# Optimization experiments

Measured on AMD Instinct MI355X. Metric: run time of the kernel, lower is better.

## Reference

```python
import jax, jax.numpy as jnp
import numpy as np

ALPHA, BETA, LAMB, GAMMA = 1.0, 1.0, 1e-4, 1.0
K_NN, TAU = 50, 0.1
EPS = 1e-8


def _sqdist(A, B):
    # ||a - b||^2, clamped at 0 like the torch code
    d2 = (A * A).sum(1)[:, None] + (B * B).sum(1)[None, :] - 2.0 * (A @ B.T)
    return jnp.maximum(d2, 0.0)


def _mmd(s, t):
    comb = jnp.concatenate([s, t], axis=0)
    sigma_sq = jax.lax.stop_gradient(jnp.median(_sqdist(comb, comb))) / 2.0
    sigma_sq = jnp.where(sigma_sq < 1e-6, jnp.float32(1.0), sigma_sq)
    g = 1.0 / (sigma_sq + EPS)
    kxx = jnp.exp(-g * _sqdist(s, s)).mean()
    kyy = jnp.exp(-g * _sqdist(t, t)).mean()
    kxy = jnp.exp(-g * _sqdist(s, t)).mean()
    return jnp.maximum(kxx + kyy - 2.0 * kxy, 0.0)


def setup_inputs() -> dict:
    key = jax.random.key(0)
    ks = jax.random.split(key, 8)
    B, d, N, Nq, K = 256, 128, 200000, 10000, K_NN
    q_batch = jax.random.normal(ks[0], (B, d), jnp.float32)
    X = jax.random.normal(ks[1], (N, d), jnp.float32)
    W = jax.random.normal(ks[2], (d, d), jnp.float32) * (1.0 / np.sqrt(d))
    b = jnp.zeros((d,), jnp.float32)
    pre_weights = jax.random.uniform(ks[3], (Nq, K), jnp.float32)
    pre_weights = pre_weights / pre_weights.sum(1, keepdims=True)
    pre_indices = jax.random.randint(ks[4], (Nq, K), 0, N)
    q_indices = jax.random.randint(ks[5], (B,), 0, Nq)
    idx = jax.random.randint(ks[6], (B,), 0, N)
    return {"q_batch": q_batch, "X": X, "W": W, "b": b,
            "pre_weights": pre_weights, "pre_indices": pre_indices,
            "q_indices": q_indices, "idx": idx}


def reference(q_batch, X, W, b, pre_weights, pre_indices, q_indices, idx):
    Tq = q_batch @ W.T + b                                   # model(q_batch), Linear(d, d)
    # ---- MMD between mapped queries and a random database batch ----
    loss_dist = _mmd(Tq, X[idx])
    # ---- exact KNN (faiss IndexFlatL2 equivalent) on detached embeddings ----
    d2_all = _sqdist(jax.lax.stop_gradient(Tq), X)           # [B, N]
    _, post_idx = jax.lax.top_k(-d2_all, K_NN)               # [B, K] nearest neighbors
    Xn = X[post_idx]                                         # [B, K, d]
    l2 = ((Tq[:, None, :] - Xn) ** 2).sum(-1)                # [B, K] (grad flows here)
    post_w = jax.nn.softmax(-l2 / TAU, axis=1)
    # ---- union-KL, vectorized over batch (exact torch.unique semantics) ----
    pre_i = pre_indices[q_indices]                           # [B, K]
    pre_w = pre_weights[q_indices]                           # [B, K]
    cat = jnp.concatenate([pre_i, post_idx], axis=1)         # [B, 2K]
    # multiplicity of each id within the concatenated list -> collapse duplicates
    mult = (cat[:, :, None] == cat[:, None, :]).sum(-1).astype(jnp.float32)  # [B, 2K]
    p_raw = jnp.einsum('bmk,bk->bm',
                       (cat[:, :, None] == pre_i[:, None, :]).astype(jnp.float32), pre_w)
    q_raw = jnp.einsum('bmk,bk->bm',
                       (cat[:, :, None] == post_idx[:, None, :]).astype(jnp.float32), post_w)
    p_c = jnp.maximum(p_raw, EPS)
    q_c = jnp.maximum(q_raw, EPS)
    p = p_c / (p_c / mult).sum(1, keepdims=True)             # normalize over union
    q = q_c / (q_c / mult).sum(1, keepdims=True)
    kl = ((p * (jnp.log(p) - jnp.log(q))) / mult).sum(1)     # KL(p || q) per sample
    loss_knn = kl.mean()
    # ---- L2 regularization of model params & anchor loss ----
    loss_reg = 0.5 * ((W ** 2).sum() + (b ** 2).sum())
    loss_anchor = ((Tq - q_batch) ** 2).sum(1).mean()
    total = ALPHA * loss_dist + BETA * loss_knn + LAMB * loss_reg + GAMMA * loss_anchor
    return jnp.stack([total, loss_dist, loss_knn, loss_anchor])
```

## Files before the change

kernel.cpp:

```cpp
#include <hip/hip_runtime.h>
#include <cstdint>

#define D 128
#define NPTS 200000
#define KNN 50
#define CAP 8192
#define NS 8192
#define SLACK 2.0f
#define BAND 4.0f
#define EB 2048

#define OFF_ACC    0
#define OFF_SEL    256
#define OFF_CNT    1024
#define OFF_HIST0  17408
#define OFF_HIST12 148480
#define ZERO_BYTES 214016
#define OFF_COMB   214016
#define OFF_D2     476160
#define OFF_XN     1524736
#define OFF_SAMP   2324736
#define OFF_EBUF   2324736
#define OFF_THR    10713344
#define OFF_CANDI  10714368
#define OFF_SCO    19102976
#define OFF_TQSW   27491584
#define OFF_XBF    27557120
#define OFF_ANCP   78757120
#define OFF_WREGP  78758144
#define OFF_BCNT   78758400
#define OFF_KSA    78774272

typedef __attribute__((ext_vector_type(8))) short bf16x8;
typedef __attribute__((ext_vector_type(4))) float f32x4;
typedef const __attribute__((address_space(1))) void* gas_p;
typedef __attribute__((address_space(3))) void* las_p;

__device__ __forceinline__ unsigned fkey(float f) {
    unsigned u = __float_as_uint(f);
    return u ^ ((unsigned)((int)u >> 31) | 0x80000000u);
}

__device__ __forceinline__ void stage8k(const unsigned short* __restrict__ g,
                                        unsigned short* l, int w, int lane)
{
    #pragma unroll
    for (int j = 0; j < 2; j++) {
        const unsigned short* gp = g + j * 2048 + w * 512 + lane * 8;
        unsigned short* lp = l + j * 2048 + w * 512;
        __builtin_amdgcn_global_load_lds((gas_p)gp, (las_p)lp, 16, 0, 0);
    }
}

__global__ void k_phase1(const float* __restrict__ q, const float* __restrict__ X,
                         const float* __restrict__ W, const float* __restrict__ bb,
                         const int* __restrict__ idx, float* __restrict__ comb,
                         unsigned short* __restrict__ tqsw, unsigned short* __restrict__ xbf,
                         float* __restrict__ xn, float* __restrict__ ancp,
                         float* __restrict__ wregp, float* __restrict__ wszero)
{
    const int blk = blockIdx.x, t = threadIdx.x;
    if (blk < 12500) {
        __shared__ float xr4[4][16];
        const int lr = t & 15;
// ... 110 lines not shown
            const int r = (ck * 2 + tt) * 16 + lr;
            float xnv = xn[r];
            bf16x8 bfr[4];
            #pragma unroll
            for (int ks = 0; ks < 4; ks++)
                bfr[ks] = *(const bf16x8*)(sb + tt * 2048 + ks * 512 + lane * 8);
            f32x4 acc4[4];
            #pragma unroll
            for (int i = 0; i < 4; i++) acc4[i] = (f32x4){0.f, 0.f, 0.f, 0.f};
            #pragma unroll
            for (int ks = 0; ks < 4; ks++)
                #pragma unroll
                for (int i = 0; i < 4; i++)
                    acc4[i] = __builtin_amdgcn_mfma_f32_16x16x32_bf16(a[i][ks], bfr[ks], acc4[i], 0, 0, 0);
            #pragma unroll
            for (int i = 0; i < 4; i++)
                #pragma unroll
                for (int reg = 0; reg < 4; reg++) {
                    int qq = w * 64 + i * 16 + quad * 4 + reg;
                    samp[qq * NS + r] = xnv - 2.f * acc4[i][reg];
                }
        }
    }
}

__global__ void k_h1thr(const float* __restrict__ D2w, unsigned* __restrict__ hist12,
                        const unsigned* __restrict__ hist0, unsigned* __restrict__ sel,
                        const float* __restrict__ samp, float* __restrict__ thr)
{
    __shared__ unsigned buf[8192];
    __shared__ unsigned bins[4096];
    __shared__ unsigned part[256];
    __shared__ unsigned selll[4];
    __shared__ unsigned wred[4];
    const int t = threadIdx.x;
    if (blockIdx.x < 256) {
        unsigned s = 0;
        #pragma unroll
        for (int m = 0; m < 16; m++) {
            int bin = t * 16 + m;
            unsigned bs = 0;
            #pragma unroll
            for (int sh = 0; sh < 8; sh++) bs += hist0[bin * 8 + sh];
            bins[bin] = bs;
            s += bs;
        }
        part[t] = s;
        for (int m = t; m < 8192; m += 256) buf[m] = 0;
        __syncthreads();
        if (t == 0) {
            for (int tg = 0; tg < 2; tg++) {
                unsigned r = tg ? 131072u : 131071u;
                int c = 0;
                while (part[c] <= r) { r -= part[c]; c++; }
                int b = c * 16;
                while (bins[b] <= r) { r -= bins[b]; b++; }
                selll[2 * tg] = (unsigned)b; selll[2 * tg + 1] = r;
            }
            if (blockIdx.x == 0) {
                sel[0] = selll[0]; sel[1] = selll[1]; sel[2] = selll[2]; sel[3] = selll[3];
            }
        }
        __syncthreads();
        unsigned p0 = selll[0], p1 = selll[2];
        const int e0 = blockIdx.x * 1024;
        for (int m = 0; m < 4; m++) {
            unsigned key = __float_as_uint(D2w[e0 + m * 256 + t]);
            if ((key >> 20) == p0) atomicAdd(&buf[(key >> 8) & 0xFFFu], 1u);
            if ((key >> 20) == p1) atomicAdd(&buf[4096 + ((key >> 8) & 0xFFFu)], 1u);
        }
        __syncthreads();
        for (int m = t; m < 8192; m += 256) { unsigned v = buf[m]; if (v) atomicAdd(&hist12[m], v); }
    } else {
        const int q = blockIdx.x - 256;
        unsigned kreg[32];
        #pragma unroll
        for (int i = 0; i < 32; i++) kreg[i] = fkey(samp[q * NS + i * 256 + t]);
        unsigned v = 0;
        for (int bit = 31; bit >= 0; bit--) {
            unsigned trial = v | (1u << bit);
            unsigned c = 0;
            #pragma unroll
            for (int i = 0; i < 32; i++) c += (kreg[i] < trial) ? 1u : 0u;
            #pragma unroll
            for (int off = 32; off > 0; off >>= 1) c += __shfl_down(c, off);
            if ((t & 63) == 0) wred[t >> 6] = c;
            __syncthreads();
            unsigned total = wred[0] + wred[1] + wred[2] + wred[3];
            __syncthreads();
            if (total <= (unsigned)(KNN - 1)) v = trial;
        }
        if (t == 0) {
            unsigned orig = (v & 0x80000000u) ? (v ^ 0x80000000u) : ~v;
            thr[q] = __uint_as_float(orig) + SLACK;
        }
    }
}

#define FILT_BODY(SBUF)                                                              \
    do {                                                                             \
        _Pragma("unroll")                                                            \
        for (int tt = 0; tt < 2; tt++) {                                             \
            const int r = (ck * 2 + tt) * 16 + lr;                                   \
            float xnv = xn[r];                                                       \
            bf16x8 bv[4];                                                            \
            _Pragma("unroll")                                                        \
            for (int ks2 = 0; ks2 < 4; ks2++)                                        \
                bv[ks2] = *(const bf16x8*)(SBUF + tt * 2048 + ks2 * 512 + lane * 8); \
            f32x4 acc4[4];                                                           \
            _Pragma("unroll")                                                        \
            for (int i = 0; i < 4; i++) acc4[i] = (f32x4){0.f, 0.f, 0.f, 0.f};       \
            _Pragma("unroll")                                                        \
            for (int ks2 = 0; ks2 < 4; ks2++)                                        \
                _Pragma("unroll")                                                    \
                for (int i = 0; i < 4; i++)                                          \
                    acc4[i] = __builtin_amdgcn_mfma_f32_16x16x32_bf16(a[i][ks2], bv[ks2], acc4[i], 0, 0, 0); \
            _Pragma("unroll")                                                        \
            for (int i = 0; i < 4; i++)                                              \
                _Pragma("unroll")                                                    \
                for (int reg = 0; reg < 4; reg++) {                                  \
                    float s = xnv - 2.f * acc4[i][reg];                              \
                    if (s <= th_r[i][reg]) {                                         \
                        unsigned qq = (unsigned)(w * 64 + i * 16 + quad * 4 + reg);  \
                        unsigned p = atomicAdd(&lcnt, 1u);                           \
                        if (p < 1024u) { lbuf[p] = (qq << 18) | (unsigned)r; lsco[p] = fkey(s); } \
                        else {                                                       \
                            unsigned dd2 = gbase + p;                                \
                            if (dd2 < EB) { eb[dd2] = (qq << 18) | (unsigned)r; ebs[dd2] = fkey(s); } \
                        }                                                            \
                    }                                                                \
                }                                                                    \
        }                                                                            \
    } while (0)

__global__ __launch_bounds__(256) void k_filt2(const unsigned short* __restrict__ tqsw,
    const unsigned short* __restrict__ xbf, const float* __restrict__ xn,
    const float* __restrict__ thr, unsigned* __restrict__ ebuf, unsigned* __restrict__ esco,
    unsigned* __restrict__ bcnt, const float* __restrict__ D2w,
    unsigned* __restrict__ hist12, unsigned* __restrict__ sel)
{
    if (blockIdx.x >= 1024) {
        __shared__ unsigned h2c[512];
        __shared__ unsigned part2[256];
        __shared__ unsigned pfx[2];
        __shared__ unsigned rr[2];
        const int t = threadIdx.x;
        for (int tg = 0; tg < 2; tg++) {
            const unsigned* hh = hist12 + tg * 4096;
            unsigned s = 0;
            for (int m = 0; m < 16; m++) s += hh[t * 16 + m];
            part2[t] = s;
            __syncthreads();
            if (t == 0) {
                unsigned r = sel[1 + 2 * tg];
                int c = 0;
                while (part2[c] <= r) { r -= part2[c]; c++; }
                int b = c * 16;
                while (hh[b] <= r) { r -= hh[b]; b++; }
                pfx[tg] = (sel[2 * tg] << 12) | (unsigned)b;
                rr[tg] = r;
            }
            __syncthreads();
        }
        if (blockIdx.x == 1024 && t == 0) {
            sel[4] = pfx[0]; sel[5] = rr[0]; sel[6] = pfx[1]; sel[7] = rr[1];
        }
        h2c[t] = 0; h2c[256 + t] = 0;
        __syncthreads();
        unsigned p0 = pfx[0], p1 = pfx[1];
        const int e0 = (blockIdx.x - 1024) * 1024;
        for (int m = 0; m < 4; m++) {
            unsigned key = __float_as_uint(D2w[e0 + m * 256 + t]);
            if ((key >> 8) == p0) atomicAdd(&h2c[key & 0xFFu], 1u);
            if ((key >> 8) == p1) atomicAdd(&h2c[256 + (key & 0xFFu)], 1u);
        }
        __syncthreads();
        unsigned* gp = hist12 + 8192;
        unsigned v0 = h2c[t], v1 = h2c[256 + t];
        if (v0) atomicAdd(&gp[t], v0);
        if (v1) atomicAdd(&gp[4096 + t], v1);
        return;
    }
    __shared__ unsigned short sbA[4096];
    __shared__ unsigned short sbB[4096];
    __shared__ unsigned lbuf[1024];
    __shared__ unsigned lsco[1024];
    __shared__ unsigned lcnt;
    __shared__ unsigned gbase;
    const int t = threadIdx.x;
    const int w = t >> 6, lane = t & 63;
    const int lr = lane & 15, quad = lane >> 4;
    unsigned* eb  = ebuf + (unsigned)blockIdx.x * EB;
    unsigned* ebs = esco + (unsigned)blockIdx.x * EB;
    bf16x8 a[4][4];
    #pragma unroll
    for (int i = 0; i < 4; i++)
        #pragma unroll
        for (int ks = 0; ks < 4; ks++)
            a[i][ks] = *(const bf16x8*)(tqsw + (w * 4 + i) * 2048 + ks * 512 + lane * 8);
    float th_r[4][4];
    #pragma unroll
    for (int i = 0; i < 4; i++)
        #pragma unroll
        for (int reg = 0; reg < 4; reg++)
            th_r[i][reg] = thr[w * 64 + i * 16 + quad * 4 + reg];
    int ck = blockIdx.x;
    bool phaseA = true;
    if (t == 0) { lcnt = 0; gbase = 0; }
    stage8k(xbf + (long)ck * 4096, sbA, w, lane);
    __syncthreads();
    while (true) {
        const int ckn = ck + 1024;
        const bool has = ckn < 6250;
        if (phaseA) {
            if (has) stage8k(xbf + (long)ckn * 4096, sbB, w, lane);
            FILT_BODY(sbA);
        } else {
            if (has) stage8k(xbf + (long)ckn * 4096, sbA, w, lane);
            FILT_BODY(sbB);
        }
        __syncthreads();
        unsigned n = lcnt;
        if (!has || n >= 512u) {
            unsigned nf = (n < 1024u) ? n : 1024u;
            unsigned gb = gbase;
            for (unsigned m = t; m < nf; m += 256) {
                unsigned d = gb + m;
                if (d < EB) { eb[d] = lbuf[m]; ebs[d] = lsco[m]; }
            }
            __syncthreads();
            if (t == 0) { gbase = gb + n; lcnt = 0; }
            __syncthreads();
        }
        if (!has) break;
        ck = ckn; phaseA = !phaseA;
    }
    if (t == 0) bcnt[blockIdx.x] = (gbase < EB) ? gbase : EB;
}

__global__ __launch_bounds__(256) void k_scatmmd(const unsigned* __restrict__ ebuf,
    const unsigned* __restrict__ esco, const unsigned* __restrict__ bcnt,
    int* __restrict__ cand_i, unsigned* __restrict__ ksa, unsigned* __restrict__ cnt,
    const float* __restrict__ D2w, const unsigned* __restrict__ hist12,
    const unsigned* __restrict__ sel, float* __restrict__ acc)
{
    const int t = threadIdx.x;
    if (blockIdx.x >= 128) {
        __shared__ unsigned h2[512];
        __shared__ float gsh;
        __shared__ float part[12];
        const int w = t >> 6;
        h2[t] = hist12[8192 + t];
        h2[256 + t] = hist12[8192 + 4096 + t];
        __syncthreads();
        if (t == 0) {
            unsigned key[2];
            for (int tg = 0; tg < 2; tg++) {
                unsigned r = sel[5 + 2 * tg];
                const unsigned* hh = h2 + tg * 256;
                int b = 0;
                while (hh[b] <= r) { r -= hh[b]; b++; }
                key[tg] = (sel[4 + 2 * tg] << 8) | (unsigned)b;
            }
            float med = 0.5f * (__uint_as_float(key[0]) + __uint_as_float(key[1]));
            float ssq = 0.5f * med;
            if (ssq < 1e-6f) ssq = 1.0f;
            gsh = 1.0f / (ssq + 1e-8f);
        }
        __syncthreads();
        const float g = gsh;
        float s[3] = {0.f, 0.f, 0.f};
        const int e0 = (blockIdx.x - 128) * 1024;
        #pragma unroll
        for (int m = 0; m < 4; m++) {
            int e = e0 + m * 256 + t;
            int i = e >> 9, j = e & 511;
            float v = expf(-g * D2w[e]);
            int qd = (i < 256) ? ((j < 256) ? 0 : 2) : ((j < 256) ? 2 : 1);
            s[qd] += v;
        }
        #pragma unroll
        for (int c = 0; c < 3; c++) {
            float x = s[c];
            #pragma unroll
            for (int off = 32; off > 0; off >>= 1) x += __shfl_down(x, off);
            if ((t & 63) == 0) part[w * 3 + c] = x;
        }
        __syncthreads();
        if (t == 0)
            for (int c = 0; c < 3; c++)
                atomicAdd(&acc[2 + c], part[c] + part[3 + c] + part[6 + c] + part[9 + c]);
        return;
    }
    __shared__ unsigned hist[256];
    __shared__ unsigned startp[256];
    const int b0 = blockIdx.x * 8;
    hist[t] = 0;
    __syncthreads();
    for (int b = b0; b < b0 + 8; b++) {
        unsigned n = bcnt[b];
        const unsigned* e = ebuf + (unsigned)b * EB;
        for (unsigned m = t; m < n; m += 256)
            atomicAdd(&hist[e[m] >> 18], 1u);
    }
    __syncthreads();
    unsigned c = hist[t];
    if (c) {
        unsigned base = atomicAdd(&cnt[t * 16], c);
        startp[t] = ((unsigned)t << 13) + base;
    }
    __syncthreads();
    for (int b = b0; b < b0 + 8; b++) {
        unsigned n = bcnt[b];
        const unsigned* e = ebuf + (unsigned)b * EB;
        const unsigned* e2 = esco + (unsigned)b * EB;
        for (unsigned m = t; m < n; m += 256) {
            unsigned ent = e[m];
            unsigned sk = e2[m];
            unsigned qq = ent >> 18;
            unsigned pos = atomicAdd(&startp[qq], 1u);
            if (pos < ((qq + 1u) << 13)) { cand_i[pos] = (int)(ent & 0x3FFFFu); ksa[pos] = sk; }
        }
    }
}

__global__ __launch_bounds__(1024) void k_rp(const float* __restrict__ comb,
                        const float* __restrict__ X,
                        const int* __restrict__ cand_i, const unsigned* __restrict__ ksa,
                        const unsigned* __restrict__ cnt,
                        const int* __restrict__ pri,
                        const float* __restrict__ prw, const int* __restrict__ qix,
                        const float* __restrict__ xn,
                        float* __restrict__ acc, unsigned* __restrict__ sel,
                        const float* __restrict__ ancp, const float* __restrict__ wregp,
                        float* __restrict__ out)
{
    __shared__ unsigned ks[CAP];
    __shared__ unsigned hs[4096];
    __shared__ unsigned wsum[16];
    __shared__ float qrow[D];
    __shared__ unsigned scnt, wpos, eqn, bsel, vsh;
    __shared__ int eq[64];
    __shared__ int pidx[KNN];
    __shared__ float l2s[KNN];
    __shared__ float pw[KNN];
    __shared__ int ci[100];
    __shared__ float pwv[50], qwv[50];
    __shared__ float pterm[100], qterm[100], kterm[100];
    __shared__ float Sp, Sq;
    const int q = blockIdx.x, t = threadIdx.x;
    if (t < D) qrow[t] = comb[q * D + t];
    if (t == 0) { wpos = 0; eqn = 0; scnt = 0; bsel = 4095u; }
    unsigned nn = cnt[q * 16];
    const int n = (nn < (unsigned)CAP) ? (int)nn : CAP;
    for (int m = t; m < 4096; m += 1024) hs[m] = 0;
    __syncthreads();
    for (int m = t; m < n; m += 1024) {
        unsigned kv = ksa[q * CAP + m];
        ks[m] = kv;
        atomicAdd(&hs[kv >> 20], 1u);
    }
    __syncthreads();
    int kk = KNN - 1; if (kk > n - 1) kk = n - 1;
    {
        unsigned h0 = hs[t * 4], h1 = hs[t * 4 + 1], h2 = hs[t * 4 + 2], h3 = hs[t * 4 + 3];
        unsigned c4 = h0 + h1 + h2 + h3;
        unsigned sc = c4;
        #pragma unroll
        for (int off = 1; off < 64; off <<= 1) {
            unsigned o = __shfl_up(sc, off);
            if ((t & 63) >= off) sc += o;
        }
        if ((t & 63) == 63) wsum[t >> 6] = sc;
        __syncthreads();
        unsigned wbase = 0;
        #pragma unroll
        for (int i = 0; i < 16; i++) wbase += (i < (t >> 6)) ? wsum[i] : 0u;
        unsigned excl = wbase + sc - c4;
        unsigned kku = (unsigned)kk;
        if (c4 > 0 && kku >= excl && kku < excl + c4) {
            unsigned cum = excl;
            int b = t * 4;
            if (kku >= cum + h0) { cum += h0; b++;
                if (kku >= cum + h1) { cum += h1; b++;
                    if (kku >= cum + h2) { cum += h2; b++; } } }
            bsel = (unsigned)b;
        }
    }
    __syncthreads();
    unsigned vkeep;
    {
        unsigned b = bsel;
        if (b >= 4095u) vkeep = 0xFFFFFFFFu;
        else {
            unsigned bk = (b + 1u) << 20;
            unsigned bf = (bk & 0x80000000u) ? (bk ^ 0x80000000u) : ~bk;
            vkeep = fkey(__uint_as_float(bf) + BAND);
        }
    }
    int* sidx = (int*)hs;
    unsigned* eks = hs + 2048;
    for (int m = t; m < n; m += 1024) {
        if (ks[m] <= vkeep) {
            unsigned p = atomicAdd(&scnt, 1u);
            if (p < 2048u) sidx[p] = cand_i[q * CAP + m];
        }
    }
    __syncthreads();
    const bool cpath = (scnt <= 2048u);
    const int ns = cpath ? (int)scnt : n;
    const int g = t >> 3, j = t & 7;
    if (cpath) {
        for (int m = g; m < ns; m += 128) {
            int r = sidx[m];
            const float4* xr = (const float4*)(X + (long)r * D);
            float s = 0.f;
            #pragma unroll
            for (int p = 0; p < 4; p++) {
                float4 xv = xr[j * 4 + p];
                float4 qv = *(const float4*)&qrow[(j * 4 + p) * 4];
                s = fmaf(xv.x, qv.x, fmaf(xv.y, qv.y, fmaf(xv.z, qv.z, fmaf(xv.w, qv.w, s))));
            }
            s += __shfl_down(s, 4); s += __shfl_down(s, 2); s += __shfl_down(s, 1);
            if (j == 0) eks[m] = fkey(xn[r] - 2.f * s);
        }
    } else {
        for (int m = g; m < ns; m += 128) {
            int r = cand_i[q * CAP + m];
            const float4* xr = (const float4*)(X + (long)r * D);
            float s = 0.f;
            #pragma unroll
            for (int p = 0; p < 4; p++) {
                float4 xv = xr[j * 4 + p];
                float4 qv = *(const float4*)&qrow[(j * 4 + p) * 4];
                s = fmaf(xv.x, qv.x, fmaf(xv.y, qv.y, fmaf(xv.z, qv.z, fmaf(xv.w, qv.w, s))));
            }
            s += __shfl_down(s, 4); s += __shfl_down(s, 2); s += __shfl_down(s, 1);
            if (j == 0) ks[m] = fkey(xn[r] - 2.f * s);
        }
    }
    __syncthreads();
    int kk2 = KNN - 1; if (kk2 > ns - 1) kk2 = ns - 1;
    if (t < 64) {
        unsigned v = 0;
        for (int bit = 31; bit >= 0; bit--) {
            unsigned trial = v | (1u << bit);
            unsigned c = 0;
            for (int m = t; m < ns; m += 64) {
                unsigned kv2 = cpath ? eks[m] : ks[m];
                c += (kv2 < trial) ? 1u : 0u;
            }
            #pragma unroll
            for (int off = 32; off > 0; off >>= 1) c += __shfl_xor(c, off);
            if (c <= (unsigned)kk2) v = trial;
        }
        if (t == 0) vsh = v;
    }
    __syncthreads();
    const unsigned v = vsh;
    for (int m = t; m < ns; m += 1024) {
        unsigned kv = cpath ? eks[m] : ks[m];
        int r = cpath ? sidx[m] : cand_i[q * CAP + m];
        if (kv < v) {
            unsigned p = atomicAdd(&wpos, 1u);
            pidx[p] = r;
        } else if (kv == v) {
            unsigned p = atomicAdd(&eqn, 1u);
            if (p < 64) eq[p] = r;
        }
    }
    __syncthreads();
    if (t == 0) {
        int c1 = (int)wpos, need = KNN - c1;
        int ne = (eqn < 64u) ? (int)eqn : 64;
        for (int a = 0; a < ne; a++)
            for (int b2 = a + 1; b2 < ne; b2++)
                if (eq[b2] < eq[a]) { int tmp = eq[a]; eq[a] = eq[b2]; eq[b2] = tmp; }
        for (int a = 0; a < need && a < ne; a++) pidx[c1 + a] = eq[a];
    }
    __syncthreads();
    for (int nb = g; nb < KNN; nb += 128) {
        long r = pidx[nb];
        const float4* xr = (const float4*)(X + r * D);
        float s = 0.f;
        #pragma unroll
        for (int p = 0; p < 4; p++) {
            float4 xv = xr[j * 4 + p];
            float4 qv = *(const float4*)&qrow[(j * 4 + p) * 4];
            float d0 = qv.x - xv.x, d1 = qv.y - xv.y, d2 = qv.z - xv.z, d3 = qv.w - xv.w;
            s += d0 * d0 + d1 * d1 + d2 * d2 + d3 * d3;
        }
        s += __shfl_down(s, 4); s += __shfl_down(s, 2); s += __shfl_down(s, 1);
        if (j == 0) l2s[nb] = s;
    }
    int qi = qix[q];
    if (t >= 128 && t < 178) { int k = t - 128; ci[k] = pri[qi * 50 + k]; pwv[k] = prw[qi * 50 + k]; }
    __syncthreads();
    if (t < 64) {
        float logit = (t < KNN) ? (-l2s[t] * 10.0f) : -3.4e38f;
        float m = logit;
        #pragma unroll
        for (int off = 32; off > 0; off >>= 1) m = fmaxf(m, __shfl_down(m, off));
        m = __shfl(m, 0);
        float e = (t < KNN) ? expf(logit - m) : 0.f;
        float ss = e;
        #pragma unroll
        for (int off = 32; off > 0; off >>= 1) ss += __shfl_down(ss, off);
        ss = __shfl(ss, 0);
        if (t < KNN) pw[t] = e / ss;
    }
    __syncthreads();
    if (t < 50) { ci[50 + t] = pidx[t]; qwv[t] = pw[t]; }
    __syncthreads();
    float pc = 0.f, qc = 0.f, mult = 0.f;
    if (t < 100) {
        int c = ci[t];
        float pr = 0.f, qr = 0.f;
        for (int k = 0; k < 50; k++) {
            bool m1 = (c == ci[k]); bool m2 = (c == ci[50 + k]);
            mult += (m1 ? 1.f : 0.f) + (m2 ? 1.f : 0.f);
            pr += m1 ? pwv[k] : 0.f;
            qr += m2 ? qwv[k] : 0.f;
        }
        pc = fmaxf(pr, 1e-8f); qc = fmaxf(qr, 1e-8f);
        pterm[t] = pc / mult; qterm[t] = qc / mult;
    }
    __syncthreads();
    if (t == 0) { float a = 0.f, b2 = 0.f; for (int m = 0; m < 100; m++) { a += pterm[m]; b2 += qterm[m]; } Sp = a; Sq = b2; }
    __syncthreads();
    if (t < 100) {
        float p = pc / Sp, qq2 = qc / Sq;
        kterm[t] = (p * (logf(p) - logf(qq2))) / mult;
    }
    __syncthreads();
    if (t == 0) {
        float s = 0.f;
        for (int m = 0; m < 100; m++) s += kterm[m];
        atomicAdd(&acc[1], s);
        __threadfence();
        unsigned old = atomicAdd(&sel[15], 1u);
        if (old == 255u) {
            __threadfence();
            float lknn = atomicAdd(&acc[1], 0.f) / 256.f;
            float reg = 0.f;
            #pragma unroll
            for (int m = 0; m < 4; m++) reg += wregp[m];
            reg *= 0.5f;
            float anc = 0.f;
            for (int m = 0; m < 256; m++) anc += ancp[m];
            float lanc = anc / 256.f;
            float kxx = acc[2] / 65536.f, kyy = acc[3] / 65536.f, kxy = acc[4] / 131072.f;
            float ld = fmaxf(kxx + kyy - 2.f * kxy, 0.f);
            out[0] = ld + lknn + 1e-4f * reg + lanc;
            out[1] = ld; out[2] = lknn; out[3] = lanc;
        }
    }
}

extern "C" void kernel_launch(void* const* d_in, const int* in_sizes, int n_in,
                              void* d_out, int out_size, void* d_ws, size_t ws_size,
                              hipStream_t stream)
{
    (void)in_sizes; (void)n_in; (void)out_size; (void)ws_size;
    const float* q   = (const float*)d_in[0];
    const float* X   = (const float*)d_in[1];
    const float* W   = (const float*)d_in[2];
    const float* bb  = (const float*)d_in[3];
    const float* prw = (const float*)d_in[4];
    const int*   pri = (const int*)d_in[5];
    const int*   qix = (const int*)d_in[6];
    const int*   idx = (const int*)d_in[7];
    float* out = (float*)d_out;
    char* ws = (char*)d_ws;
    float*    acc   = (float*)(ws + OFF_ACC);
    unsigned* sel   = (unsigned*)(ws + OFF_SEL);
    unsigned* cnt   = (unsigned*)(ws + OFF_CNT);
    unsigned* hist0 = (unsigned*)(ws + OFF_HIST0);
    unsigned* hist12= (unsigned*)(ws + OFF_HIST12);
    float*    comb  = (float*)(ws + OFF_COMB);
    float*    D2w   = (float*)(ws + OFF_D2);
    float*    xn    = (float*)(ws + OFF_XN);
    float*    samp  = (float*)(ws + OFF_SAMP);
    float*    thr   = (float*)(ws + OFF_THR);
    int*      cix   = (int*)(ws + OFF_CANDI);
    unsigned* ebuf  = (unsigned*)(ws + OFF_EBUF);
    unsigned* esco  = (unsigned*)(ws + OFF_SCO);
    unsigned* bcnt  = (unsigned*)(ws + OFF_BCNT);
    unsigned* ksa   = (unsigned*)(ws + OFF_KSA);
    unsigned short* tqsw = (unsigned short*)(ws + OFF_TQSW);
    unsigned short* xbf  = (unsigned short*)(ws + OFF_XBF);
    float*    ancp  = (float*)(ws + OFF_ANCP);
    float*    wregp = (float*)(ws + OFF_WREGP);

    hipLaunchKernelGGL(k_phase1,  dim3(12764),   dim3(256), 0, stream, q, X, W, bb, idx, comb, tqsw, xbf, xn, ancp, wregp, acc);
    hipLaunchKernelGGL(k_d2m,     dim3(1280),    dim3(256), 0, stream, comb, D2w, hist0, tqsw, xbf, xn, samp);
    hipLaunchKernelGGL(k_h1thr,   dim3(512),     dim3(256), 0, stream, D2w, hist12, hist0, sel, samp, thr);
    hipLaunchKernelGGL(k_filt2,   dim3(1280),    dim3(256), 0, stream, tqsw, xbf, xn, thr, ebuf, esco, bcnt, D2w, hist12, sel);
    hipLaunchKernelGGL(k_scatmmd, dim3(384),     dim3(256), 0, stream, ebuf, esco, bcnt, cix, ksa, cnt, D2w, hist12, sel, acc);
    hipLaunchKernelGGL(k_rp,      dim3(256),     dim3(1024), 0, stream, comb, X, cix, ksa, cnt, pri, prw, qix, xn, acc, sel, ancp, wregp, out);
}
```

Measured before the change: 336.7 us.

## Write filter candidates into per-block per-query segments and drop scatter kernel

Result: no change. 343.3 us (+1.9%).

```diff
diff --git a/kernel.cpp b/kernel.cpp
--- a/kernel.cpp
+++ b/kernel.cpp
@@ -8,7 +8,8 @@
 #define NS 8192
 #define SLACK 2.0f
 #define BAND 4.0f
-#define EB 2048
+#define SEGCAP 64
+#define NFB 1024
 
 #define OFF_ACC    0
 #define OFF_SEL    256
@@ -20,16 +21,13 @@
 #define OFF_D2     476160
 #define OFF_XN     1524736
 #define OFF_SAMP   2324736
-#define OFF_EBUF   2324736
 #define OFF_THR    10713344
-#define OFF_CANDI  10714368
-#define OFF_SCO    19102976
 #define OFF_TQSW   27491584
 #define OFF_XBF    27557120
 #define OFF_ANCP   78757120
 #define OFF_WREGP  78758144
-#define OFF_BCNT   78758400
-#define OFF_KSA    78774272
+#define OFF_CKSEG  78774272
+#define OFF_SEGC   212992000
 
 typedef __attribute__((ext_vector_type(8))) short bf16x8;
 typedef __attribute__((ext_vector_type(4))) float f32x4;
@@ -206,7 +204,6 @@
     __shared__ unsigned bins[4096];
     __shared__ unsigned part[256];
     __shared__ unsigned selll[4];
-    __shared__ unsigned wred[4];
     const int t = threadIdx.x;
     if (blockIdx.x < 256) {
         unsigned s = 0;
@@ -247,26 +244,30 @@
         for (int m = t; m < 8192; m += 256) { unsigned v = buf[m]; if (v) atomicAdd(&hist12[m], v); }
     } else {
         const int q = blockIdx.x - 256;
-        unsigned kreg[32];
-        #pragma unroll
-        for (int i = 0; i < 32; i++) kreg[i] = fkey(samp[q * NS + i * 256 + t]);
-        unsigned v = 0;
-        for (int bit = 31; bit >= 0; bit--) {
-            unsigned trial = v | (1u << bit);
-            unsigned c = 0;
-            #pragma unroll
-            for (int i = 0; i < 32; i++) c += (kreg[i] < trial) ? 1u : 0u;
-            #pragma unroll
-            for (int off = 32; off > 0; off >>= 1) c += __shfl_down(c, off);
-            if ((t & 63) == 0) wred[t >> 6] = c;
-            __syncthreads();
-            unsigned total = wred[0] + wred[1] + wred[2] + wred[3];
-            __syncthreads();
-            if (total <= (unsigned)(KNN - 1)) v = trial;
-        }
+        for (int m = t; m < 4096; m += 256) buf[m] = 0;
+        __syncthreads();
+        for (int m = t; m < NS; m += 256)
+            atomicAdd(&buf[fkey(samp[q * NS + m]) >> 20], 1u);
+        __syncthreads();
+        unsigned s = 0;
+        #pragma unroll
+        for (int m2 = 0; m2 < 16; m2++) s += buf[t * 16 + m2];
+        part[t] = s;
+        __syncthreads();
         if (t == 0) {
-            unsigned orig = (v & 0x80000000u) ? (v ^ 0x80000000u) : ~v;
-            thr[q] = __uint_as_float(orig) + SLACK;
+            unsigned r = (unsigned)(KNN - 1);
+            int c = 0;
+            while (part[c] <= r) { r -= part[c]; c++; }
+            int b = c * 16;
+            while (buf[b] <= r) { r -= buf[b]; b++; }
+            float up;
+            if (b >= 4095) up = 3.4e38f;
+            else {
+                unsigned bk = (unsigned)(b + 1) << 20;
+                unsigned bf = (bk & 0x80000000u) ? (bk ^ 0x80000000u) : ~bk;
+                up = __uint_as_float(bf);
+            }
+            thr[q] = up + SLACK;
         }
     }
 }
@@ -296,12 +297,9 @@
                     float s = xnv - 2.f * acc4[i][reg];                              \
                     if (s <= th_r[i][reg]) {                                         \
                         unsigned qq = (unsigned)(w * 64 + i * 16 + quad * 4 + reg);  \
-                        unsigned p = atomicAdd(&lcnt, 1u);                           \
-                        if (p < 1024u) { lbuf[p] = (qq << 18) | (unsigned)r; lsco[p] = fkey(s); } \
-                        else {                                                       \
-                            unsigned dd2 = gbase + p;                                \
-                            if (dd2 < EB) { eb[dd2] = (qq << 18) | (unsigned)r; ebs[dd2] = fkey(s); } \
-                        }                                                            \
+                        unsigned slot = atomicAdd(&segcL[qq], 1u);                   \
+                        if (slot < (unsigned)SEGCAP)                                 \
+                            cks[qq * SEGCAP + slot] = make_uint2((unsigned)r, fkey(s)); \
                     }                                                                \
                 }                                                                    \
         }                                                                            \
@@ -309,9 +307,8 @@
 
 __global__ __launch_bounds__(256) void k_filt2(const unsigned short* __restrict__ tqsw,
     const unsigned short* __restrict__ xbf, const float* __restrict__ xn,
-    const float* __restrict__ thr, unsigned* __restrict__ ebuf, unsigned* __restrict__ esco,
-    unsigned* __restrict__ bcnt, const float* __restrict__ D2w,
-    unsigned* __restrict__ hist12, unsigned* __restrict__ sel)
+    const float* __restrict__ thr, uint2* __restrict__ ckseg, unsigned* __restrict__ segcnt,
+    const float* __restrict__ D2w, unsigned* __restrict__ hist12, unsigned* __restrict__ sel)
 {
     if (blockIdx.x >= 1024) {
         __shared__ unsigned h2c[512];
@@ -357,15 +354,12 @@
     }
     __shared__ unsigned short sbA[4096];
     __shared__ unsigned short sbB[4096];
-    __shared__ unsigned lbuf[1024];
-    __shared__ unsigned lsco[1024];
-    __shared__ unsigned lcnt;
-    __shared__ unsigned gbase;
+    __shared__ unsigned segcL[256];
     const int t = threadIdx.x;
     const int w = t >> 6, lane = t & 63;
     const int lr = lane & 15, quad = lane >> 4;
-    unsigned* eb  = ebuf + (unsigned)blockIdx.x * EB;
-    unsigned* ebs = esco + (unsigned)blockIdx.x * EB;
+    uint2* cks = ckseg + (unsigned)blockIdx.x * 256u * SEGCAP;
+    segcL[t] = 0;
     bf16x8 a[4][4];
     #pragma unroll
     for (int i = 0; i < 4; i++)
@@ -380,7 +374,6 @@
             th_r[i][reg] = thr[w * 64 + i * 16 + quad * 4 + reg];
     int ck = blockIdx.x;
     bool phaseA = true;
-    if (t == 0) { lcnt = 0; gbase = 0; }
     stage8k(xbf + (long)ck * 4096, sbA, w, lane);
     __syncthreads();
     while (true) {
@@ -394,326 +387,298 @@
             FILT_BODY(sbB);
         }
         __syncthreads();
-        unsigned n = lcnt;
-        if (!has || n >= 512u) {
-            unsigned nf = (n < 1024u) ? n : 1024u;
-            unsigned gb = gbase;
-            for (unsigned m = t; m < nf; m += 256) {
-                unsigned d = gb + m;
-                if (d < EB) { eb[d] = lbuf[m]; ebs[d] = lsco[m]; }
-            }
-            __syncthreads();
-            if (t == 0) { gbase = gb + n; lcnt = 0; }
-            __syncthreads();
-        }
         if (!has) break;
         ck = ckn; phaseA = !phaseA;
     }
-    if (t == 0) bcnt[blockIdx.x] = (gbase < EB) ? gbase : EB;
+    unsigned c = segcL[t];
+    segcnt[(unsigned)blockIdx.x * 256u + (unsigned)t] = (c < (unsigned)SEGCAP) ? c : (unsigned)SEGCAP;
 }
 
-__global__ __launch_bounds__(256) void k_scatmmd(const unsigned* __restrict__ ebuf,
-    const unsigned* __restrict__ esco, const unsigned* __restrict__ bcnt,
-    int* __restrict__ cand_i, unsigned* __restrict__ ksa, unsigned* __restrict__ cnt,
-    const float* __restrict__ D2w, const unsigned* __restrict__ hist12,
-    const unsigned* __restrict__ sel, float* __restrict__ acc)
+__global__ __launch_bounds__(1024) void k_rp(const float* __restrict__ comb,
+                        const float* __restrict__ X,
+                        const uint2* __restrict__ ckseg, const unsigned* __restrict__ segcnt,
+                        const int* __restrict__ pri,
+                        const float* __restrict__ prw, const int* __restrict__ qix,
+                        const float* __restrict__ xn, const float* __restrict__ D2w,
+                        const unsigned* __restrict__ hist12,
+                        float* __restrict__ acc, unsigned* __restrict__ sel,
+                        const float* __restrict__ ancp, const float* __restrict__ wregp,
+                        float* __restrict__ out)
 {
-    const int t = threadIdx.x;
-    if (blockIdx.x >= 128) {
-        __shared__ unsigned h2[512];
-        __shared__ float gsh;
-        __shared__ float part[12];
-        const int w = t >> 6;
-        h2[t] = hist12[8192 + t];
-        h2[256 + t] = hist12[8192 + 4096 + t];
+    __shared__ __align__(16) char smraw[85504];
+    const int b = blockIdx.x, t = threadIdx.x;
+    const int w = t >> 6, lane = t & 63;
+    if (b >= 256) {
+        unsigned* h2 = (unsigned*)smraw;
+        float* gshp = (float*)(smraw + 2048);
+        float* partf = (float*)(smraw + 2064);
+        if (t < 256) h2[t] = hist12[8192 + t];
+        else if (t < 512) h2[t] = hist12[8192 + 4096 + (t - 256)];
         __syncthreads();
         if (t == 0) {
             unsigned key[2];
             for (int tg = 0; tg < 2; tg++) {
                 unsigned r = sel[5 + 2 * tg];
                 const unsigned* hh = h2 + tg * 256;
-                int b = 0;
-                while (hh[b] <= r) { r -= hh[b]; b++; }
-                key[tg] = (sel[4 + 2 * tg] << 8) | (unsigned)b;
+                int bb2 = 0;
+                while (hh[bb2] <= r) { r -= hh[bb2]; bb2++; }
+                key[tg] = (sel[4 + 2 * tg] << 8) | (unsigned)bb2;
             }
             float med = 0.5f * (__uint_as_float(key[0]) + __uint_as_float(key[1]));
             float ssq = 0.5f * med;
             if (ssq < 1e-6f) ssq = 1.0f;
-            gsh = 1.0f / (ssq + 1e-8f);
-        }
-        __syncthreads();
-        const float g = gsh;
-        float s[3] = {0.f, 0.f, 0.f};
-        const int e0 = (blockIdx.x - 128) * 1024;
-        #pragma unroll
-        for (int m = 0; m < 4; m++) {
-            int e = e0 + m * 256 + t;
-            int i = e >> 9, j = e & 511;
-            float v = expf(-g * D2w[e]);
-            int qd = (i < 256) ? ((j < 256) ? 0 : 2) : ((j < 256) ? 2 : 1);
-            s[qd] += v;
-        }
-        #pragma unroll
-        for (int c = 0; c < 3; c++) {
-            float x = s[c];
-            #pragma unroll
-            for (int off = 32; off > 0; off >>= 1) x += __shfl_down(x, off);
-            if ((t & 63) == 0) part[w * 3 + c] = x;
-        }
-        __syncthreads();
-        if (t == 0)
-            for (int c = 0; c < 3; c++)
-                atomicAdd(&acc[2 + c], part[c] + part[3 + c] + part[6 + c] + part[9 + c]);
-        return;
-    }
-    __shared__ unsigned hist[256];
-    __shared__ unsigned startp[256];
-    const int b0 = blockIdx.x * 8;
-    hist[t] = 0;
-    __syncthreads();
-    for (int b = b0; b < b0 + 8; b++) {
-        unsigned n = bcnt[b];
-        const unsigned* e = ebuf + (unsigned)b * EB;
-        for (unsigned m = t; m < n; m += 256)
-            atomicAdd(&hist[e[m] >> 18], 1u);
-    }
-    __syncthreads();
-    unsigned c = hist[t];
-    if (c) {
-        unsigned base = atomicAdd(&cnt[t * 16], c);
-        startp[t] = ((unsigned)t << 13) + base;
-    }
-    __syncthreads();
-    for (int b = b0; b < b0 + 8; b++) {
-        unsigned n = bcnt[b];
-        const unsigned* e = ebuf + (unsigned)b * EB;
-        const unsigned* e2 = esco + (unsigned)b * EB;
-        for (unsigned m = t; m < n; m += 256) {
-            unsigned ent = e[m];
-            unsigned sk = e2[m];
-            unsigned qq = ent >> 18;
-            unsigned pos = atomicAdd(&startp[qq], 1u);
-            if (pos < ((qq + 1u) << 13)) { cand_i[pos] = (int)(ent & 0x3FFFFu); ksa[pos] = sk; }
-        }
-    }
-}
-
-__global__ __launch_bounds__(1024) void k_rp(const float* __restrict__ comb,
-                        const float* __restrict__ X,
-                        const int* __restrict__ cand_i, const unsigned* __restrict__ ksa,
-                        const unsigned* __restrict__ cnt,
-                        const int* __restrict__ pri,
-                        const float* __restrict__ prw, const int* __restrict__ qix,
-                        const float* __restrict__ xn,
-                        float* __restrict__ acc, unsigned* __restrict__ sel,
-                        const float* __restrict__ ancp, const float* __restrict__ wregp,
-                        float* __restrict__ out)
-{
-    __shared__ unsigned ks[CAP];
-    __shared__ unsigned hs[4096];
-    __shared__ unsigned wsum[16];
-    __shared__ float qrow[D];
-    __shared__ unsigned scnt, wpos, eqn, bsel, vsh;
-    __shared__ int eq[64];
-    __shared__ int pidx[KNN];
-    __shared__ float l2s[KNN];
-    __shared__ float pw[KNN];
-    __shared__ int ci[100];
-    __shared__ float pwv[50], qwv[50];
-    __shared__ float pterm[100], qterm[100], kterm[100];
-    __shared__ float Sp, Sq;
-    const int q = blockIdx.x, t = threadIdx.x;
-    if (t < D) qrow[t] = comb[q * D + t];
-    if (t == 0) { wpos = 0; eqn = 0; scnt = 0; bsel = 4095u; }
-    unsigned nn = cnt[q * 16];
-    const int n = (nn < (unsigned)CAP) ? (int)nn : CAP;
-    for (int m = t; m < 4096; m += 1024) hs[m] = 0;
-    __syncthreads();
-    for (int m = t; m < n; m += 1024) {
-        unsigned kv = ksa[q * CAP + m];
-        ks[m] = kv;
-        atomicAdd(&hs[kv >> 20], 1u);
-    }
-    __syncthreads();
-    int kk = KNN - 1; if (kk > n - 1) kk = n - 1;
-    {
-        unsigned h0 = hs[t * 4], h1 = hs[t * 4 + 1], h2 = hs[t * 4 + 2], h3 = hs[t * 4 + 3];
-        unsigned c4 = h0 + h1 + h2 + h3;
-        unsigned sc = c4;
+            gshp[0] = 1.0f / (ssq + 1e-8f);
+        }
+        __syncthreads();
+        const float g = gshp[0];
+        const int e = (b - 256) * 1024 + t;
+        const int i2 = e >> 9, j2 = e & 511;
+        float v = expf(-g * D2w[e]);
+        int qd = (i2 < 256) ? ((j2 < 256) ? 0 : 2) : ((j2 < 256) ? 2 : 1);
+        float s0 = (qd == 0) ? v : 0.f, s1 = (qd == 1) ? v : 0.f, s2 = (qd == 2) ? v : 0.f;
+        #pragma unroll
+        for (int off = 32; off > 0; off >>= 1) {
+            s0 += __shfl_down(s0, off);
+            s1 += __shfl_down(s1, off);
+            s2 += __shfl_down(s2, off);
+        }
+        if (lane == 0) { partf[w * 3 + 0] = s0; partf[w * 3 + 1] = s1; partf[w * 3 + 2] = s2; }
+        __syncthreads();
+        if (t == 0) {
+            float a0 = 0.f, a1 = 0.f, a2 = 0.f;
+            #pragma unroll
+            for (int i = 0; i < 16; i++) { a0 += partf[i * 3]; a1 += partf[i * 3 + 1]; a2 += partf[i * 3 + 2]; }
+            atomicAdd(&acc[2], a0); atomicAdd(&acc[3], a1); atomicAdd(&acc[4], a2);
+        }
+    } else {
+        const int q = b;
+        unsigned* ks   = (unsigned*)smraw;
+        unsigned* cid  = (unsigned*)(smraw + 32768);
+        unsigned* hs   = (unsigned*)(smraw + 65536);
+        unsigned* wsum = (unsigned*)(smraw + 81920);
+        float* qrow    = (float*)(smraw + 81984);
+        unsigned* ctr  = (unsigned*)(smraw + 82496);
+        int* eq        = (int*)(smraw + 82516);
+        int* pidx      = (int*)(smraw + 82772);
+        float* l2s     = (float*)(smraw + 82972);
+        float* pw      = (float*)(smraw + 83172);
+        int* ci        = (int*)(smraw + 83372);
+        float* pwv     = (float*)(smraw + 83772);
+        float* qwv     = (float*)(smraw + 83972);
+        float* pterm   = (float*)(smraw + 84172);
+        float* qterm   = (float*)(smraw + 84572);
+        float* kterm   = (float*)(smraw + 84972);
+        float* SpSq    = (float*)(smraw + 85372);
+        if (t < D) qrow[t] = comb[q * D + t];
+        if (t == 0) { ctr[0] = 0; ctr[1] = 0; ctr[2] = 0; ctr[3] = 4095u; }
+        for (int m = t; m < 4096; m += 1024) hs[m] = 0;
+        unsigned cb = segcnt[(unsigned)t * 256u + (unsigned)q];
+        unsigned sc = cb;
         #pragma unroll
         for (int off = 1; off < 64; off <<= 1) {
             unsigned o = __shfl_up(sc, off);
-            if ((t & 63) >= off) sc += o;
-        }
-        if ((t & 63) == 63) wsum[t >> 6] = sc;
-        __syncthreads();
-        unsigned wbase = 0;
-        #pragma unroll
-        for (int i = 0; i < 16; i++) wbase += (i < (t >> 6)) ? wsum[i] : 0u;
-        unsigned excl = wbase + sc - c4;
-        unsigned kku = (unsigned)kk;
-        if (c4 > 0 && kku >= excl && kku < excl + c4) {
-            unsigned cum = excl;
-            int b = t * 4;
-            if (kku >= cum + h0) { cum += h0; b++;
-                if (kku >= cum + h1) { cum += h1; b++;
-                    if (kku >= cum + h2) { cum += h2; b++; } } }
-            bsel = (unsigned)b;
-        }
-    }
-    __syncthreads();
-    unsigned vkeep;
-    {
-        unsigned b = bsel;
-        if (b >= 4095u) vkeep = 0xFFFFFFFFu;
-        else {
-            unsigned bk = (b + 1u) << 20;
-            unsigned bf = (bk & 0x80000000u) ? (bk ^ 0x80000000u) : ~bk;
-            vkeep = fkey(__uint_as_float(bf) + BAND);
-        }
-    }
-    int* sidx = (int*)hs;
-    unsigned* eks = hs + 2048;
-    for (int m = t; m < n; m += 1024) {
-        if (ks[m] <= vkeep) {
-            unsigned p = atomicAdd(&scnt, 1u);
-            if (p < 2048u) sidx[p] = cand_i[q * CAP + m];
-        }
-    }
-    __syncthreads();
-    const bool cpath = (scnt <= 2048u);
-    const int ns = cpath ? (int)scnt : n;
-    const int g = t >> 3, j = t & 7;
-    if (cpath) {
-        for (int m = g; m < ns; m += 128) {
-            int r = sidx[m];
-            const float4* xr = (const float4*)(X + (long)r * D);
+            if (lane >= off) sc += o;
+        }
+        if (lane == 63) wsum[w] = sc;
+        __syncthreads();
+        unsigned wbase = 0, total = 0;
+        #pragma unroll
+        for (int i = 0; i < 16; i++) { total += wsum[i]; wbase += (i < w) ? wsum[i] : 0u; }
+        unsigned excl = wbase + sc - cb;
+        const int n = (total < (unsigned)CAP) ? (int)total : CAP;
+        {
+            const uint2* seg = ckseg + ((unsigned)t * 256u + (unsigned)q) * SEGCAP;
+            for (unsigned s2 = 0; s2 < cb; s2++) {
+                unsigned d = excl + s2;
+                if (d < (unsigned)CAP) { uint2 e2 = seg[s2]; ks[d] = e2.y; cid[d] = e2.x; }
+            }
+        }
+        __syncthreads();
+        for (int m = t; m < n; m += 1024) atomicAdd(&hs[ks[m] >> 20], 1u);
+        __syncthreads();
+        int kk = KNN - 1; if (kk > n - 1) kk = n - 1;
+        {
+            unsigned h0 = hs[t * 4], h1 = hs[t * 4 + 1], h2 = hs[t * 4 + 2], h3 = hs[t * 4 + 3];
+            unsigned c4 = h0 + h1 + h2 + h3;
+            unsigned sc2 = c4;
+            #pragma unroll
+            for (int off = 1; off < 64; off <<= 1) {
+                unsigned o = __shfl_up(sc2, off);
+                if (lane >= off) sc2 += o;
+            }
+            if (lane == 63) wsum[w] = sc2;
+            __syncthreads();
+            unsigned wbase2 = 0;
+            #pragma unroll
+            for (int i = 0; i < 16; i++) wbase2 += (i < w) ? wsum[i] : 0u;
+            unsigned excl2 = wbase2 + sc2 - c4;
+            unsigned kku = (unsigned)kk;
+            if (c4 > 0 && kku >= excl2 && kku < excl2 + c4) {
+                unsigned cum = excl2;
+                int bb3 = t * 4;
+                if (kku >= cum + h0) { cum += h0; bb3++;
+                    if (kku >= cum + h1) { cum += h1; bb3++;
+                        if (kku >= cum + h2) { cum += h2; bb3++; } } }
+                ctr[3] = (unsigned)bb3;
+            }
+        }
+        __syncthreads();
+        unsigned vkeep;
+        {
+            unsigned bb4 = ctr[3];
+            if (bb4 >= 4095u) vkeep = 0xFFFFFFFFu;
+            else {
+                unsigned bk = (bb4 + 1u) << 20;
+                unsigned bf = (bk & 0x80000000u) ? (bk ^ 0x80000000u) : ~bk;
+                vkeep = fkey(__uint_as_float(bf) + BAND);
+            }
+        }
+        int* sidx = (int*)hs;
+        unsigned* eks = hs + 2048;
+        for (int m = t; m < n; m += 1024) {
+            if (ks[m] <= vkeep) {
+                unsigned p = atomicAdd(&ctr[0], 1u);
+                if (p < 2048u) sidx[p] = (int)cid[m];
+            }
+        }
+        __syncthreads();
+        const unsigned scnt = ctr[0];
+        const bool cpath = (scnt <= 2048u);
+        const int ns = cpath ? (int)scnt : n;
+        const int g2 = t >> 3, j = t & 7;
+        if (cpath) {
+            for (int m = g2; m < ns; m += 128) {
+                int r = sidx[m];
+                const float4* xr = (const float4*)(X + (long)r * D);
+                float s = 0.f;
+                #pragma unroll
+                for (int p = 0; p < 4; p++) {
+                    float4 xv = xr[j * 4 + p];
+                    float4 qv = *(const float4*)&qrow[(j * 4 + p) * 4];
+                    s = fmaf(xv.x, qv.x, fmaf(xv.y, qv.y, fmaf(xv.z, qv.z, fmaf(xv.w, qv.w, s))));
+                }
+                s += __shfl_down(s, 4); s += __shfl_down(s, 2); s += __shfl_down(s, 1);
+                if (j == 0) eks[m] = fkey(xn[r] - 2.f * s);
+            }
+        } else {
+            for (int m = g2; m < ns; m += 128) {
+                int r = (int)cid[m];
+                const float4* xr = (const float4*)(X + (long)r * D);
+                float s = 0.f;
+                #pragma unroll
+                for (int p = 0; p < 4; p++) {
+                    float4 xv = xr[j * 4 + p];
+                    float4 qv = *(const float4*)&qrow[(j * 4 + p) * 4];
+                    s = fmaf(xv.x, qv.x, fmaf(xv.y, qv.y, fmaf(xv.z, qv.z, fmaf(xv.w, qv.w, s))));
+                }
+                s += __shfl_down(s, 4); s += __shfl_down(s, 2); s += __shfl_down(s, 1);
+                if (j == 0) ks[m] = fkey(xn[r] - 2.f * s);
+            }
+        }
+        __syncthreads();
+        int kk2 = KNN - 1; if (kk2 > ns - 1) kk2 = ns - 1;
+        if (t < 64) {
+            unsigned v2 = 0;
+            for (int bit = 31; bit >= 0; bit--) {
+                unsigned trial = v2 | (1u << bit);
+                unsigned c = 0;
+                for (int m = t; m < ns; m += 64) {
+                    unsigned kv2 = cpath ? eks[m] : ks[m];
+                    c += (kv2 < trial) ? 1u : 0u;
+                }
+                #pragma unroll
+                for (int off = 32; off > 0; off >>= 1) c += __shfl_xor(c, off);
+                if (c <= (unsigned)kk2) v2 = trial;
+            }
+            if (t == 0) ctr[4] = v2;
+        }
+        __syncthreads();
+        const unsigned v = ctr[4];
+        for (int m = t; m < ns; m += 1024) {
+            unsigned kv = cpath ? eks[m] : ks[m];
+            int r = cpath ? sidx[m] : (int)cid[m];
+            if (kv < v) {
+                unsigned p = atomicAdd(&ctr[1], 1u);
+                pidx[p] = r;
+            } else if (kv == v) {
+                unsigned p = atomicAdd(&ctr[2], 1u);
+                if (p < 64) eq[p] = r;
+            }
+        }
+        __syncthreads();
+        if (t == 0) {
+            int c1 = (int)ctr[1], need = KNN - c1;
+            int ne = (ctr[2] < 64u) ? (int)ctr[2] : 64;
+            for (int a = 0; a < ne; a++)
+                for (int b2 = a + 1; b2 < ne; b2++)
+                    if (eq[b2] < eq[a]) { int tmp = eq[a]; eq[a] = eq[b2]; eq[b2] = tmp; }
+            for (int a = 0; a < need && a < ne; a++) pidx[c1 + a] = eq[a];
+        }
+        __syncthreads();
+        for (int nb = g2; nb < KNN; nb += 128) {
+            long r = pidx[nb];
+            const float4* xr = (const float4*)(X + r * D);
             float s = 0.f;
             #pragma unroll
             for (int p = 0; p < 4; p++) {
                 float4 xv = xr[j * 4 + p];
                 float4 qv = *(const float4*)&qrow[(j * 4 + p) * 4];
-                s = fmaf(xv.x, qv.x, fmaf(xv.y, qv.y, fmaf(xv.z, qv.z, fmaf(xv.w, qv.w, s))));
+                float d0 = qv.x - xv.x, d1 = qv.y - xv.y, d2 = qv.z - xv.z, d3 = qv.w - xv.w;
+                s += d0 * d0 + d1 * d1 + d2 * d2 + d3 * d3;
             }
             s += __shfl_down(s, 4); s += __shfl_down(s, 2); s += __shfl_down(s, 1);
-            if (j == 0) eks[m] = fkey(xn[r] - 2.f * s);
-        }
-    } else {
-        for (int m = g; m < ns; m += 128) {
-            int r = cand_i[q * CAP + m];
-            const float4* xr = (const float4*)(X + (long)r * D);
+            if (j == 0) l2s[nb] = s;
+        }
+        int qi = qix[q];
+        if (t >= 128 && t < 178) { int k = t - 128; ci[k] = pri[qi * 50 + k]; pwv[k] = prw[qi * 50 + k]; }
+        __syncthreads();
+        if (t < 64) {
+            float logit = (t < KNN) ? (-l2s[t] * 10.0f) : -3.4e38f;
+            float m = logit;
+            #pragma unroll
+            for (int off = 32; off > 0; off >>= 1) m = fmaxf(m, __shfl_down(m, off));
+            m = __shfl(m, 0);
+            float e = (t < KNN) ? expf(logit - m) : 0.f;
+            float ss = e;
+            #pragma unroll
+            for (int off = 32; off > 0; off >>= 1) ss += __shfl_down(ss, off);
+            ss = __shfl(ss, 0);
+            if (t < KNN) pw[t] = e / ss;
+        }
+        __syncthreads();
+        if (t < 50) { ci[50 + t] = pidx[t]; qwv[t] = pw[t]; }
+        __syncthreads();
+        float pc = 0.f, qc = 0.f, mult = 0.f;
+        if (t < 100) {
+            int c = ci[t];
+            float pr = 0.f, qr = 0.f;
+            for (int k = 0; k < 50; k++) {
+                bool m1 = (c == ci[k]); bool m2 = (c == ci[50 + k]);
+                mult += (m1 ? 1.f : 0.f) + (m2 ? 1.f : 0.f);
+                pr += m1 ? pwv[k] : 0.f;
+                qr += m2 ? qwv[k] : 0.f;
+            }
+            pc = fmaxf(pr, 1e-8f); qc = fmaxf(qr, 1e-8f);
+            pterm[t] = pc / mult; qterm[t] = qc / mult;
+        }
+        __syncthreads();
+        if (t == 0) { float a = 0.f, b2 = 0.f; for (int m = 0; m < 100; m++) { a += pterm[m]; b2 += qterm[m]; } SpSq[0] = a; SpSq[1] = b2; }
+        __syncthreads();
+        if (t < 100) {
+            float p = pc / SpSq[0], qq2 = qc / SpSq[1];
+            kterm[t] = (p * (logf(p) - logf(qq2))) / mult;
+        }
+        __syncthreads();
+        if (t == 0) {
             float s = 0.f;
-            #pragma unroll
-            for (int p = 0; p < 4; p++) {
-                float4 xv = xr[j * 4 + p];
-                float4 qv = *(const float4*)&qrow[(j * 4 + p) * 4];
-                s = fmaf(xv.x, qv.x, fmaf(xv.y, qv.y, fmaf(xv.z, qv.z, fmaf(xv.w, qv.w, s))));
-            }
-            s += __shfl_down(s, 4); s += __shfl_down(s, 2); s += __shfl_down(s, 1);
-            if (j == 0) ks[m] = fkey(xn[r] - 2.f * s);
+            for (int m = 0; m < 100; m++) s += kterm[m];
+            atomicAdd(&acc[1], s);
         }
     }
-    __syncthreads();
-    int kk2 = KNN - 1; if (kk2 > ns - 1) kk2 = ns - 1;
-    if (t < 64) {
-        unsigned v = 0;
-        for (int bit = 31; bit >= 0; bit--) {
-            unsigned trial = v | (1u << bit);
-            unsigned c = 0;
-            for (int m = t; m < ns; m += 64) {
-                unsigned kv2 = cpath ? eks[m] : ks[m];
-                c += (kv2 < trial) ? 1u : 0u;
-            }
-            #pragma unroll
-            for (int off = 32; off > 0; off >>= 1) c += __shfl_xor(c, off);
-            if (c <= (unsigned)kk2) v = trial;
-        }
-        if (t == 0) vsh = v;
-    }
-    __syncthreads();
-    const unsigned v = vsh;
-    for (int m = t; m < ns; m += 1024) {
-        unsigned kv = cpath ? eks[m] : ks[m];
-        int r = cpath ? sidx[m] : cand_i[q * CAP + m];
-        if (kv < v) {
-            unsigned p = atomicAdd(&wpos, 1u);
-            pidx[p] = r;
-        } else if (kv == v) {
-            unsigned p = atomicAdd(&eqn, 1u);
-            if (p < 64) eq[p] = r;
-        }
-    }
-    __syncthreads();
     if (t == 0) {
-        int c1 = (int)wpos, need = KNN - c1;
-        int ne = (eqn < 64u) ? (int)eqn : 64;
-        for (int a = 0; a < ne; a++)
-            for (int b2 = a + 1; b2 < ne; b2++)
-                if (eq[b2] < eq[a]) { int tmp = eq[a]; eq[a] = eq[b2]; eq[b2] = tmp; }
-        for (int a = 0; a < need && a < ne; a++) pidx[c1 + a] = eq[a];
-    }
-    __syncthreads();
-    for (int nb = g; nb < KNN; nb += 128) {
-        long r = pidx[nb];
-        const float4* xr = (const float4*)(X + r * D);
-        float s = 0.f;
-        #pragma unroll
-        for (int p = 0; p < 4; p++) {
-            float4 xv = xr[j * 4 + p];
-            float4 qv = *(const float4*)&qrow[(j * 4 + p) * 4];
-            float d0 = qv.x - xv.x, d1 = qv.y - xv.y, d2 = qv.z - xv.z, d3 = qv.w - xv.w;
-            s += d0 * d0 + d1 * d1 + d2 * d2 + d3 * d3;
-        }
-        s += __shfl_down(s, 4); s += __shfl_down(s, 2); s += __shfl_down(s, 1);
-        if (j == 0) l2s[nb] = s;
-    }
-    int qi = qix[q];
-    if (t >= 128 && t < 178) { int k = t - 128; ci[k] = pri[qi * 50 + k]; pwv[k] = prw[qi * 50 + k]; }
-    __syncthreads();
-    if (t < 64) {
-        float logit = (t < KNN) ? (-l2s[t] * 10.0f) : -3.4e38f;
-        float m = logit;
-        #pragma unroll
-        for (int off = 32; off > 0; off >>= 1) m = fmaxf(m, __shfl_down(m, off));
-        m = __shfl(m, 0);
-        float e = (t < KNN) ? expf(logit - m) : 0.f;
-        float ss = e;
-        #pragma unroll
-        for (int off = 32; off > 0; off >>= 1) ss += __shfl_down(ss, off);
-        ss = __shfl(ss, 0);
-        if (t < KNN) pw[t] = e / ss;
-    }
-    __syncthreads();
-    if (t < 50) { ci[50 + t] = pidx[t]; qwv[t] = pw[t]; }
-    __syncthreads();
-    float pc = 0.f, qc = 0.f, mult = 0.f;
-    if (t < 100) {
-        int c = ci[t];
-        float pr = 0.f, qr = 0.f;
-        for (int k = 0; k < 50; k++) {
-            bool m1 = (c == ci[k]); bool m2 = (c == ci[50 + k]);
-            mult += (m1 ? 1.f : 0.f) + (m2 ? 1.f : 0.f);
-            pr += m1 ? pwv[k] : 0.f;
-            qr += m2 ? qwv[k] : 0.f;
-        }
-        pc = fmaxf(pr, 1e-8f); qc = fmaxf(qr, 1e-8f);
-        pterm[t] = pc / mult; qterm[t] = qc / mult;
-    }
-    __syncthreads();
-    if (t == 0) { float a = 0.f, b2 = 0.f; for (int m = 0; m < 100; m++) { a += pterm[m]; b2 += qterm[m]; } Sp = a; Sq = b2; }
-    __syncthreads();
-    if (t < 100) {
-        float p = pc / Sp, qq2 = qc / Sq;
-        kterm[t] = (p * (logf(p) - logf(qq2))) / mult;
-    }
-    __syncthreads();
-    if (t == 0) {
-        float s = 0.f;
-        for (int m = 0; m < 100; m++) s += kterm[m];
-        atomicAdd(&acc[1], s);
         __threadfence();
         unsigned old = atomicAdd(&sel[15], 1u);
-        if (old == 255u) {
+        if (old == 511u) {
             __threadfence();
             float lknn = atomicAdd(&acc[1], 0.f) / 256.f;
             float reg = 0.f;
@@ -748,7 +713,6 @@
     char* ws = (char*)d_ws;
     float*    acc   = (float*)(ws + OFF_ACC);
     unsigned* sel   = (unsigned*)(ws + OFF_SEL);
-    unsigned* cnt   = (unsigned*)(ws + OFF_CNT);
     unsigned* hist0 = (unsigned*)(ws + OFF_HIST0);
     unsigned* hist12= (unsigned*)(ws + OFF_HIST12);
     float*    comb  = (float*)(ws + OFF_COMB);
@@ -756,20 +720,16 @@
     float*    xn    = (float*)(ws + OFF_XN);
     float*    samp  = (float*)(ws + OFF_SAMP);
     float*    thr   = (float*)(ws + OFF_THR);
-    int*      cix   = (int*)(ws + OFF_CANDI);
-    unsigned* ebuf  = (unsigned*)(ws + OFF_EBUF);
-    unsigned* esco  = (unsigned*)(ws + OFF_SCO);
-    unsigned* bcnt  = (unsigned*)(ws + OFF_BCNT);
-    unsigned* ksa   = (unsigned*)(ws + OFF_KSA);
+    uint2*    ckseg = (uint2*)(ws + OFF_CKSEG);
+    unsigned* segcnt= (unsigned*)(ws + OFF_SEGC);
     unsigned short* tqsw = (unsigned short*)(ws + OFF_TQSW);
     unsigned short* xbf  = (unsigned short*)(ws + OFF_XBF);
     float*    ancp  = (float*)(ws + OFF_ANCP);
     float*    wregp = (float*)(ws + OFF_WREGP);
 
-    hipLaunchKernelGGL(k_phase1,  dim3(12764),   dim3(256), 0, stream, q, X, W, bb, idx, comb, tqsw, xbf, xn, ancp, wregp, acc);
-    hipLaunchKernelGGL(k_d2m,     dim3(1280),    dim3(256), 0, stream, comb, D2w, hist0, tqsw, xbf, xn, samp);
-    hipLaunchKernelGGL(k_h1thr,   dim3(512),     dim3(256), 0, stream, D2w, hist12, hist0, sel, samp, thr);
-    hipLaunchKernelGGL(k_filt2,   dim3(1280),    dim3(256), 0, stream, tqsw, xbf, xn, thr, ebuf, esco, bcnt, D2w, hist12, sel);
-    hipLaunchKernelGGL(k_scatmmd, dim3(384),     dim3(256), 0, stream, ebuf, esco, bcnt, cix, ksa, cnt, D2w, hist12, sel, acc);
-    hipLaunchKernelGGL(k_rp,      dim3(256),     dim3(1024), 0, stream, comb, X, cix, ksa, cnt, pri, prw, qix, xn, acc, sel, ancp, wregp, out);
+    hipLaunchKernelGGL(k_phase1, dim3(12764), dim3(256),  0, stream, q, X, W, bb, idx, comb, tqsw, xbf, xn, ancp, wregp, acc);
+    hipLaunchKernelGGL(k_d2m,    dim3(1280),  dim3(256),  0, stream, comb, D2w, hist0, tqsw, xbf, xn, samp);
+    hipLaunchKernelGGL(k_h1thr,  dim3(512),   dim3(256),  0, stream, D2w, hist12, hist0, sel, samp, thr);
+    hipLaunchKernelGGL(k_filt2,  dim3(1280),  dim3(256),  0, stream, tqsw, xbf, xn, thr, ckseg, segcnt, D2w, hist12, sel);
+    hipLaunchKernelGGL(k_rp,     dim3(512),   dim3(1024), 0, stream, comb, X, ckseg, segcnt, pri, prw, qix, xn, D2w, hist12, acc, sel, ancp, wregp, out);
 }
```
